# Kernel optimization log

Measured on AMD Instinct MI355X. Metric: run time of the kernel, lower is better.

The kernel has to match this reference:

```python
import jax, jax.numpy as jnp
import numpy as np

NUM_BUOYS = 16384
TIME_STEPS = 8
FEATURE_DIM = 64
ID_EMB_DIM = 1024  # must equal gru_hidden_size for steps 4/5 to type-check
HIDDEN = 1024
NUM_EMB = 100
INPUT_SIZE = FEATURE_DIM + ID_EMB_DIM


def setup_inputs() -> dict:
    key = jax.random.key(0)
    k = jax.random.split(key, 7)
    s = 1.0 / np.sqrt(HIDDEN)
    return {
        "buoy_obs": jax.random.normal(k[0], (NUM_BUOYS, TIME_STEPS, FEATURE_DIM), jnp.float32),
        "buoy_ids": jax.random.randint(k[1], (NUM_BUOYS,), 0, NUM_EMB),
        "emb": jax.random.normal(k[2], (NUM_EMB, ID_EMB_DIM), jnp.float32),
        "W_ih": jax.random.uniform(k[3], (3 * HIDDEN, INPUT_SIZE), jnp.float32, -s, s),
        "W_hh": jax.random.uniform(k[4], (3 * HIDDEN, HIDDEN), jnp.float32, -s, s),
        "b_ih": jax.random.uniform(k[5], (3 * HIDDEN,), jnp.float32, -s, s),
        "b_hh": jax.random.uniform(k[6], (3 * HIDDEN,), jnp.float32, -s, s),
    }


def _gru_cell(x, h, W_ih, W_hh, b_ih, b_hh):
    # PyTorch GRU gate layout: [r, z, n]
    gi = x @ W_ih.T + b_ih  # (N, 3H)
    gh = h @ W_hh.T + b_hh  # (N, 3H)
    gi_r, gi_z, gi_n = jnp.split(gi, 3, axis=-1)
    gh_r, gh_z, gh_n = jnp.split(gh, 3, axis=-1)
    r = jax.nn.sigmoid(gi_r + gh_r)
    z = jax.nn.sigmoid(gi_z + gh_z)
    n = jnp.tanh(gi_n + r * gh_n)
    return (1.0 - z) * n + z * h


def reference(buoy_obs, buoy_ids, emb, W_ih, W_hh, b_ih, b_hh):
    num_buoys = buoy_obs.shape[0]
    id_emb = emb[buoy_ids]  # (N, E)
    h = jnp.zeros((num_buoys, HIDDEN), buoy_obs.dtype)
    outs = []
    # three unrolled steps: input = [obs_t, id_emb]
    for t in range(3):
        x = jnp.concatenate([buoy_obs[:, t, :], id_emb], axis=-1)
        h = _gru_cell(x, h, W_ih, W_hh, b_ih, b_hh)
        outs.append(h)
    # step 4: input = [out0, obs_1]
    x = jnp.concatenate([outs[0], buoy_obs[:, 1, :]], axis=-1)
    h = _gru_cell(x, h, W_ih, W_hh, b_ih, b_hh)
    second_out = h
    # step 5: input = [out4, obs_2]
    x = jnp.concatenate([second_out, buoy_obs[:, 2, :]], axis=-1)
    h = _gru_cell(x, h, W_ih, W_hh, b_ih, b_hh)
    # AdaptiveMaxPool1d(1) over a length-1 time axis is identity
    return h[None, :, :]  # (1, N, H)
```

## Files before the change

### kernel.cpp

```cpp
#include <hip/hip_runtime.h>
#include <hip/hip_bf16.h>


typedef __bf16 bf16_8 __attribute__((ext_vector_type(8)));
typedef float  f32_16 __attribute__((ext_vector_type(16)));

#define NBUOY 16384
#define HID   1024

__device__ __forceinline__ float sigm(float x)  { return 1.f / (1.f + __expf(-x)); }
__device__ __forceinline__ float tanh_f(float x){ return 1.f - 2.f / (1.f + __expf(2.f * x)); }

#define LOADH(a0, a1, br, bz, bn)                                        \
    a0[0] = *(const bf16_8*)(pa0); a0[1] = *(const bf16_8*)(pa0 + 512);  \
    a1[0] = *(const bf16_8*)(pa1); a1[1] = *(const bf16_8*)(pa1 + 512);  \
    br[0] = *(const bf16_8*)(pbr); br[1] = *(const bf16_8*)(pbr + 512);  \
    bz[0] = *(const bf16_8*)(pbz); bz[1] = *(const bf16_8*)(pbz + 512);  \
    bn[0] = *(const bf16_8*)(pbn); bn[1] = *(const bf16_8*)(pbn + 512);  \
    pa0 += 1024; pa1 += 1024; pbr += 1024; pbz += 1024; pbn += 1024;

#define MFMAH(a0, a1, br, bz, bn)                                                         \
    acc[0][0]  = __builtin_amdgcn_mfma_f32_32x32x16_bf16(a0[0], br[0], acc[0][0], 0,0,0); \
    acc[0][1]  = __builtin_amdgcn_mfma_f32_32x32x16_bf16(a1[0], br[0], acc[0][1], 0,0,0); \
    acc[1][0]  = __builtin_amdgcn_mfma_f32_32x32x16_bf16(a0[0], bz[0], acc[1][0], 0,0,0); \
    acc[1][1]  = __builtin_amdgcn_mfma_f32_32x32x16_bf16(a1[0], bz[0], acc[1][1], 0,0,0); \
    acc[QN][0] = __builtin_amdgcn_mfma_f32_32x32x16_bf16(a0[0], bn[0], acc[QN][0],0,0,0); \
    acc[QN][1] = __builtin_amdgcn_mfma_f32_32x32x16_bf16(a1[0], bn[0], acc[QN][1],0,0,0); \
    acc[0][0]  = __builtin_amdgcn_mfma_f32_32x32x16_bf16(a0[1], br[1], acc[0][0], 0,0,0); \
    acc[0][1]  = __builtin_amdgcn_mfma_f32_32x32x16_bf16(a1[1], br[1], acc[0][1], 0,0,0); \
    acc[1][0]  = __builtin_amdgcn_mfma_f32_32x32x16_bf16(a0[1], bz[1], acc[1][0], 0,0,0); \
    acc[1][1]  = __builtin_amdgcn_mfma_f32_32x32x16_bf16(a1[1], bz[1], acc[1][1], 0,0,0); \
    acc[QN][0] = __builtin_amdgcn_mfma_f32_32x32x16_bf16(a0[1], bn[1], acc[QN][0],0,0,0); \
    acc[QN][1] = __builtin_amdgcn_mfma_f32_32x32x16_bf16(a1[1], bn[1], acc[QN][1],0,0,0);

template<int QN, int K>
__device__ __forceinline__ void phase_direct(
    const __bf16* __restrict__ Ap, long aGS, int aG0,
    const __bf16* __restrict__ Wp, long wGS, int n0,
    f32_16 acc[4][2], int tid)
{
    const int lane = tid & 63, wid = tid >> 6;
    const int wm = wid >> 1, wn = wid & 1;
    const int nG = (n0 >> 5) + wn;

    const __bf16* pa0 = Ap + (long)(aG0 + wm * 2    ) * aGS + lane * 8;
    const __bf16* pa1 = Ap + (long)(aG0 + wm * 2 + 1) * aGS + lane * 8;
    const __bf16* pbr = Wp + (long)(      nG) * wGS + lane * 8;
    const __bf16* pbz = Wp + (long)(32  + nG) * wGS + lane * 8;
    const __bf16* pbn = Wp + (long)(64  + nG) * wGS + lane * 8;

    bf16_8 Xa0[2], Xa1[2], Xbr[2], Xbz[2], Xbn[2];
    bf16_8 Ya0[2], Ya1[2], Ybr[2], Ybz[2], Ybn[2];

    constexpr int S = K / 32;
    LOADH(Xa0, Xa1, Xbr, Xbz, Xbn)

    #pragma unroll 1
    for (int s = 0; s + 2 < S; s += 2) {
        LOADH(Ya0, Ya1, Ybr, Ybz, Ybn)
        MFMAH(Xa0, Xa1, Xbr, Xbz, Xbn)
        LOADH(Xa0, Xa1, Xbr, Xbz, Xbn)
        MFMAH(Ya0, Ya1, Ybr, Ybz, Ybn)
    }
    LOADH(Ya0, Ya1, Ybr, Ybz, Ybn)
    MFMAH(Xa0, Xa1, Xbr, Xbz, Xbn)
    MFMAH(Ya0, Ya1, Ybr, Ybz, Ybn)
}

template<int KIH, int KHH, bool USE_E, bool OUT_F32>
__global__ __launch_bounds__(256, 2)
void gru_step(const __bf16* __restrict__ Aih, long aGS,
              const __bf16* __restrict__ Wih,
              const __bf16* __restrict__ Ahh,
              const __bf16* __restrict__ Whh,
              const float*  __restrict__ E,
              const int*    __restrict__ ids,
              const float*  __restrict__ bih,
              const float*  __restrict__ bhh,
              const __bf16* __restrict__ hprev,
              void* __restrict__ outp, long sOut)
{
    const int tid  = threadIdx.x;
    const int lane = tid & 63, wid = tid >> 6;
    const int wm = wid >> 1, wn = wid & 1;
    const int l31 = lane & 31, hi = lane >> 5;
    const int m0 = blockIdx.y * 128;
    const int n0 = blockIdx.x * 64;

    f32_16 acc[4][2];
    #pragma unroll
    for (int q = 0; q < 4; ++q)
        #pragma unroll
        for (int mt = 0; mt < 2; ++mt) acc[q][mt] = (f32_16)(0.0f);

    phase_direct<2, KIH>(Aih, aGS, m0 >> 5, Wih, 34816, n0, acc, tid);
    if (KHH > 0)
        phase_direct<3, KHH>(Ahh, 34816, m0 >> 5, Whh, 32768, n0, acc, tid);

    const int col = n0 + wn * 32 + l31;
    const float bhr = bhh[col], bhz = bhh[1024 + col], bhn = bhh[2048 + col];
    float cir = 0.f, ciz = 0.f, cin = 0.f;
    if (!USE_E) { cir = bih[col]; ciz = bih[1024 + col]; cin = bih[2048 + col]; }
    const long colPk = (long)(col >> 4) * 512 + ((col >> 3) & 1) * 256 + (col & 7);

    #pragma unroll
    for (int mt = 0; mt < 2; ++mt) {
        const int g = (m0 >> 5) + wm * 2 + mt;
        #pragma unroll
        for (int reg = 0; reg < 16; ++reg) {
            const int r = 4 * hi + (reg & 3) + 8 * (reg >> 2);
            const int row = g * 32 + r;
            float er = cir, ez = ciz, en = cin;
            if (USE_E) {
                const float* Ep = E + (long)ids[row] * 3072 + col;
                er = Ep[0]; ez = Ep[1024]; en = Ep[2048];
            }
            const float rr = sigm(acc[0][mt][reg] + er + bhr);
            const float z  = sigm(acc[1][mt][reg] + ez + bhz);
            const float nn = tanh_f(acc[2][mt][reg] + en + rr * (acc[3][mt][reg] + bhn));
            float hp = 0.f;
            if (KHH > 0) hp = (float)hprev[(long)g * 34816 + r * 8 + colPk];
            const float h = (1.f - z) * nn + z * hp;
            if (OUT_F32) ((float*)outp)[(long)row * sOut + col] = h;
            else        ((__bf16*)outp)[(long)g * 34816 + r * 8 + colPk] = (__bf16)h;
        }
    }
}

__global__ void pack_W(const float* __restrict__ W, __bf16* __restrict__ P, int K)
{
    const int q  = blockIdx.x * 256 + threadIdx.x;
    const int kc = q % (K >> 3), row = q / (K >> 3);
    const float4 v0 = *(const float4*)(W + (long)row * K + kc * 8);
    const float4 v1 = *(const float4*)(W + (long)row * K + kc * 8 + 4);
    bf16_8 b;
    b[0] = (__bf16)v0.x; b[1] = (__bf16)v0.y; b[2] = (__bf16)v0.z; b[3] = (__bf16)v0.w;
    b[4] = (__bf16)v1.x; b[5] = (__bf16)v1.y; b[6] = (__bf16)v1.z; b[7] = (__bf16)v1.w;
    const long cidx = (long)(row >> 5) * (K * 4)
                    + (kc >> 1) * 64 + (kc & 1) * 32 + (row & 31);
    ((bf16_8*)P)[cidx] = b;
}

__global__ void build_obs(const float* __restrict__ obs,
                          __bf16* __restrict__ O0, __bf16* __restrict__ O1,
                          __bf16* __restrict__ O2,
                          __bf16* __restrict__ X0, __bf16* __restrict__ X1)
{
    const int q = blockIdx.x * 256 + threadIdx.x;
    const int row = q / 24, c = q % 24;
    const int t = c >> 3, kc = c & 7;
    const float4 v0 = *(const float4*)(obs + (long)row * 512 + t * 64 + kc * 8);
    const float4 v1 = *(const float4*)(obs + (long)row * 512 + t * 64 + kc * 8 + 4);
    bf16_8 b;
    b[0] = (__bf16)v0.x; b[1] = (__bf16)v0.y; b[2] = (__bf16)v0.z; b[3] = (__bf16)v0.w;
    b[4] = (__bf16)v1.x; b[5] = (__bf16)v1.y; b[6] = (__bf16)v1.z; b[7] = (__bf16)v1.w;
    const int g = row >> 5, r = row & 31;
    const long ci = (long)g * 256 + (kc >> 1) * 64 + (kc & 1) * 32 + r;
    __bf16* O = (t == 0) ? O0 : (t == 1) ? O1 : O2;
    ((bf16_8*)O)[ci] = b;
    const long cx = (long)g * 4352 + (64 + (kc >> 1)) * 64 + (kc & 1) * 32 + r;
    if (t == 1) ((bf16_8*)X0)[cx] = b;
    if (t == 2) ((bf16_8*)X1)[cx] = b;
}

#define ETILE 10
__global__ void compute_E(const float* __restrict__ emb, const float* __restrict__ Wih,
                          const float* __restrict__ bih, float* __restrict__ E)
{
    __shared__ float semb[ETILE * 1024];
    const int e0 = blockIdx.x * ETILE;
    const int j  = blockIdx.y * 256 + threadIdx.x;
    for (int i = threadIdx.x; i < ETILE * 1024; i += 256)
        semb[i] = emb[(long)(e0 + (i >> 10)) * 1024 + (i & 1023)];
    __syncthreads();
    const float* wp = Wih + (long)j * 1088 + 64;
    float a[ETILE];
    const float b = bih[j];
    #pragma unroll
    for (int t = 0; t < ETILE; ++t) a[t] = b;
    for (int k = 0; k < 1024; k += 4) {
        const float4 w = *(const float4*)(wp + k);
        #pragma unroll
        for (int t = 0; t < ETILE; ++t) {
            const float* se = semb + t * 1024 + k;
            a[t] += se[0] * w.x + se[1] * w.y + se[2] * w.z + se[3] * w.w;
        }
    }
    #pragma unroll
    for (int t = 0; t < ETILE; ++t) E[(long)(e0 + t) * 3072 + j] = a[t];
}

extern "C" void kernel_launch(void* const* d_in, const int* in_sizes, int n_in,
                              void* d_out, int out_size, void* d_ws, size_t ws_size,
                              hipStream_t stream)
{
    const float* obs = (const float*)d_in[0];
    const int*   ids = (const int*)  d_in[1];
    const float* emb = (const float*)d_in[2];
    const float* Wih = (const float*)d_in[3];
    const float* Whh = (const float*)d_in[4];
    const float* bih = (const float*)d_in[5];
    const float* bhh = (const float*)d_in[6];
    float* out = (float*)d_out;

    const size_t MB = 1 << 20;
    const size_t XB = (size_t)NBUOY * 1088 * 2;
    const size_t NEEDED = 22 * MB + 3 * XB;
    if (ws_size < NEEDED) return;

    char* ws = (char*)d_ws;
    float*  E    = (float*) ws;
    __bf16* PWih = (__bf16*)(ws + 2 * MB);
    __bf16* PWhh = (__bf16*)(ws + 9 * MB);
    __bf16* O0   = (__bf16*)(ws + 16 * MB);
    __bf16* O1   = (__bf16*)(ws + 18 * MB);
    __bf16* O2   = (__bf16*)(ws + 20 * MB);
    __bf16* X0   = (__bf16*)(ws + 22 * MB);
    __bf16* X1   = (__bf16*)(ws + 22 * MB + XB);
    __bf16* X2   = (__bf16*)(ws + 22 * MB + 2 * XB);

    dim3 blk(256);
    dim3 gridG(HID / 64, NBUOY / 128);

    pack_W<<<3072 * 1088 / 8 / 256, blk, 0, stream>>>(Wih, PWih, 1088);
    pack_W<<<3072 * 1024 / 8 / 256, blk, 0, stream>>>(Whh, PWhh, 1024);
    build_obs<<<NBUOY * 24 / 256, blk, 0, stream>>>(obs, O0, O1, O2, X0, X1);
    compute_E<<<dim3(10, 12), blk, 0, stream>>>(emb, Wih, bih, E);

    gru_step<64, 0, true, false><<<gridG, blk, 0, stream>>>(
        O0, 2048, PWih, nullptr, PWhh, E, ids, bih, bhh, nullptr, X0, 0);
    gru_step<64, 1024, true, false><<<gridG, blk, 0, stream>>>(
        O1, 2048, PWih, X0, PWhh, E, ids, bih, bhh, X0, X1, 0);
    gru_step<64, 1024, true, false><<<gridG, blk, 0, stream>>>(
        O2, 2048, PWih, X1, PWhh, E, ids, bih, bhh, X1, X2, 0);
    gru_step<1088, 1024, false, false><<<gridG, blk, 0, stream>>>(
        X0, 34816, PWih, X2, PWhh, nullptr, ids, bih, bhh, X2, X1, 0);
    gru_step<1088, 1024, false, true><<<gridG, blk, 0, stream>>>(
        X1, 34816, PWih, X1, PWhh, nullptr, ids, bih, bhh, X1, out, 1024);
}
```

Measured before the change: 970.7 us.

## Stage GEMM tiles through double-buffered LDS with async loads and larger M tile

Each wave used to load its own A and W fragments straight from global memory into registers. Now each K-slice of the A rows and the three gate weight slices is staged cooperatively into a double-buffered LDS tile using global_load_lds async copies, overlapping the next slice's loads with the current slice's MFMAs. The block grows to 512 threads covering 256 rows instead of 128, so each weight tile is reused across twice as many rows, cutting weight traffic. In exchange the kernel needs about 112 KB of LDS and a barrier per K-slice, which likely limits residency to one block per CU.

```diff
diff --git a/kernel.cpp b/kernel.cpp
--- a/kernel.cpp
+++ b/kernel.cpp
@@ -7,68 +7,70 @@
 
 #define NBUOY 16384
 #define HID   1024
-
+#define BUFSZ 28672
+
+__device__ __forceinline__ void async16(const void* g, void* l) {
+    __builtin_amdgcn_global_load_lds(
+        (const __attribute__((address_space(1))) unsigned int*)g,
+        (__attribute__((address_space(3))) unsigned int*)l, 16, 0, 0);
+}
 __device__ __forceinline__ float sigm(float x)  { return 1.f / (1.f + __expf(-x)); }
 __device__ __forceinline__ float tanh_f(float x){ return 1.f - 2.f / (1.f + __expf(2.f * x)); }
 
-#define LOADH(a0, a1, br, bz, bn)                                        \
-    a0[0] = *(const bf16_8*)(pa0); a0[1] = *(const bf16_8*)(pa0 + 512);  \
-    a1[0] = *(const bf16_8*)(pa1); a1[1] = *(const bf16_8*)(pa1 + 512);  \
-    br[0] = *(const bf16_8*)(pbr); br[1] = *(const bf16_8*)(pbr + 512);  \
-    bz[0] = *(const bf16_8*)(pbz); bz[1] = *(const bf16_8*)(pbz + 512);  \
-    bn[0] = *(const bf16_8*)(pbn); bn[1] = *(const bf16_8*)(pbn + 512);  \
-    pa0 += 1024; pa1 += 1024; pbr += 1024; pbz += 1024; pbn += 1024;
-
-#define MFMAH(a0, a1, br, bz, bn)                                                         \
-    acc[0][0]  = __builtin_amdgcn_mfma_f32_32x32x16_bf16(a0[0], br[0], acc[0][0], 0,0,0); \
-    acc[0][1]  = __builtin_amdgcn_mfma_f32_32x32x16_bf16(a1[0], br[0], acc[0][1], 0,0,0); \
-    acc[1][0]  = __builtin_amdgcn_mfma_f32_32x32x16_bf16(a0[0], bz[0], acc[1][0], 0,0,0); \
-    acc[1][1]  = __builtin_amdgcn_mfma_f32_32x32x16_bf16(a1[0], bz[0], acc[1][1], 0,0,0); \
-    acc[QN][0] = __builtin_amdgcn_mfma_f32_32x32x16_bf16(a0[0], bn[0], acc[QN][0],0,0,0); \
-    acc[QN][1] = __builtin_amdgcn_mfma_f32_32x32x16_bf16(a1[0], bn[0], acc[QN][1],0,0,0); \
-    acc[0][0]  = __builtin_amdgcn_mfma_f32_32x32x16_bf16(a0[1], br[1], acc[0][0], 0,0,0); \
-    acc[0][1]  = __builtin_amdgcn_mfma_f32_32x32x16_bf16(a1[1], br[1], acc[0][1], 0,0,0); \
-    acc[1][0]  = __builtin_amdgcn_mfma_f32_32x32x16_bf16(a0[1], bz[1], acc[1][0], 0,0,0); \
-    acc[1][1]  = __builtin_amdgcn_mfma_f32_32x32x16_bf16(a1[1], bz[1], acc[1][1], 0,0,0); \
-    acc[QN][0] = __builtin_amdgcn_mfma_f32_32x32x16_bf16(a0[1], bn[1], acc[QN][0],0,0,0); \
-    acc[QN][1] = __builtin_amdgcn_mfma_f32_32x32x16_bf16(a1[1], bn[1], acc[QN][1],0,0,0);
-
 template<int QN, int K>
-__device__ __forceinline__ void phase_direct(
+__device__ __forceinline__ void phase_tiled(
     const __bf16* __restrict__ Ap, long aGS, int aG0,
-    const __bf16* __restrict__ Wp, long wGS, int n0,
-    f32_16 acc[4][2], int tid)
+    const __bf16* __restrict__ Wp, long wGS, int nG0,
+    __bf16* ls, f32_16 acc[4][2], int tid, int& buf)
 {
     const int lane = tid & 63, wid = tid >> 6;
     const int wm = wid >> 1, wn = wid & 1;
-    const int nG = (n0 >> 5) + wn;
-
-    const __bf16* pa0 = Ap + (long)(aG0 + wm * 2    ) * aGS + lane * 8;
-    const __bf16* pa1 = Ap + (long)(aG0 + wm * 2 + 1) * aGS + lane * 8;
-    const __bf16* pbr = Wp + (long)(      nG) * wGS + lane * 8;
-    const __bf16* pbz = Wp + (long)(32  + nG) * wGS + lane * 8;
-    const __bf16* pbn = Wp + (long)(64  + nG) * wGS + lane * 8;
-
-    bf16_8 Xa0[2], Xa1[2], Xbr[2], Xbz[2], Xbn[2];
-    bf16_8 Ya0[2], Ya1[2], Ybr[2], Ybz[2], Ybn[2];
-
-    constexpr int S = K / 32;
-    LOADH(Xa0, Xa1, Xbr, Xbz, Xbn)
-
+    constexpr int NT = K / 64;
+
+    auto stage = [&](int b, int t) {
+        __bf16* dst = ls + b * BUFSZ;
+        #pragma unroll
+        for (int i = 0; i < 7; ++i) {
+            const int blk = wid * 7 + i;
+            const __bf16* src;
+            if (blk < 32) {
+                const int g = blk >> 2, kc = blk & 3;
+                src = Ap + (long)(aG0 + g) * aGS + (t * 4 + kc) * 512 + lane * 8;
+            } else {
+                const int u = blk - 32;
+                const int gate = u >> 3, ng = (u >> 2) & 1, kc = u & 3;
+                src = Wp + (long)(gate * 32 + nG0 + ng) * wGS + (t * 4 + kc) * 512 + lane * 8;
+            }
+            async16(src, dst + blk * 512);
+        }
+    };
+
+    stage(buf, 0);
     #pragma unroll 1
-    for (int s = 0; s + 2 < S; s += 2) {
-        LOADH(Ya0, Ya1, Ybr, Ybz, Ybn)
-        MFMAH(Xa0, Xa1, Xbr, Xbz, Xbn)
-        LOADH(Xa0, Xa1, Xbr, Xbz, Xbn)
-        MFMAH(Ya0, Ya1, Ybr, Ybz, Ybn)
+    for (int t = 0; t < NT; ++t) {
+        __syncthreads();
+        if (t + 1 < NT) stage(buf ^ 1, t + 1);
+        const __bf16* base = ls + buf * BUFSZ;
+        #pragma unroll
+        for (int ks = 0; ks < 4; ++ks) {
+            const bf16_8 a0 = *(const bf16_8*)(base + ((wm * 2 + 0) * 4 + ks) * 512 + lane * 8);
+            const bf16_8 a1 = *(const bf16_8*)(base + ((wm * 2 + 1) * 4 + ks) * 512 + lane * 8);
+            const bf16_8 br = *(const bf16_8*)(base + (32 + ((0 * 2 + wn) * 4 + ks)) * 512 + lane * 8);
+            const bf16_8 bz = *(const bf16_8*)(base + (32 + ((1 * 2 + wn) * 4 + ks)) * 512 + lane * 8);
+            const bf16_8 bn = *(const bf16_8*)(base + (32 + ((2 * 2 + wn) * 4 + ks)) * 512 + lane * 8);
+            acc[0][0]  = __builtin_amdgcn_mfma_f32_32x32x16_bf16(a0, br, acc[0][0], 0, 0, 0);
+            acc[0][1]  = __builtin_amdgcn_mfma_f32_32x32x16_bf16(a1, br, acc[0][1], 0, 0, 0);
+            acc[1][0]  = __builtin_amdgcn_mfma_f32_32x32x16_bf16(a0, bz, acc[1][0], 0, 0, 0);
+            acc[1][1]  = __builtin_amdgcn_mfma_f32_32x32x16_bf16(a1, bz, acc[1][1], 0, 0, 0);
+            acc[QN][0] = __builtin_amdgcn_mfma_f32_32x32x16_bf16(a0, bn, acc[QN][0], 0, 0, 0);
+            acc[QN][1] = __builtin_amdgcn_mfma_f32_32x32x16_bf16(a1, bn, acc[QN][1], 0, 0, 0);
+        }
+        buf ^= 1;
     }
-    LOADH(Ya0, Ya1, Ybr, Ybz, Ybn)
-    MFMAH(Xa0, Xa1, Xbr, Xbz, Xbn)
-    MFMAH(Ya0, Ya1, Ybr, Ybz, Ybn)
 }
 
 template<int KIH, int KHH, bool USE_E, bool OUT_F32>
-__global__ __launch_bounds__(256, 2)
+__global__ __launch_bounds__(512, 2)
 void gru_step(const __bf16* __restrict__ Aih, long aGS,
               const __bf16* __restrict__ Wih,
               const __bf16* __restrict__ Ahh,
@@ -80,11 +82,12 @@
               const __bf16* __restrict__ hprev,
               void* __restrict__ outp, long sOut)
 {
+    __shared__ __bf16 ls[2 * BUFSZ];
     const int tid  = threadIdx.x;
     const int lane = tid & 63, wid = tid >> 6;
     const int wm = wid >> 1, wn = wid & 1;
     const int l31 = lane & 31, hi = lane >> 5;
-    const int m0 = blockIdx.y * 128;
+    const int m0 = blockIdx.y * 256;
     const int n0 = blockIdx.x * 64;
 
     f32_16 acc[4][2];
@@ -93,9 +96,10 @@
         #pragma unroll
         for (int mt = 0; mt < 2; ++mt) acc[q][mt] = (f32_16)(0.0f);
 
-    phase_direct<2, KIH>(Aih, aGS, m0 >> 5, Wih, 34816, n0, acc, tid);
+    int buf = 0;
+    phase_tiled<2, KIH>(Aih, aGS, m0 >> 5, Wih, 34816, n0 >> 5, ls, acc, tid, buf);
     if (KHH > 0)
-        phase_direct<3, KHH>(Ahh, 34816, m0 >> 5, Whh, 32768, n0, acc, tid);
+        phase_tiled<3, KHH>(Ahh, 34816, m0 >> 5, Whh, 32768, n0 >> 5, ls, acc, tid, buf);
 
     const int col = n0 + wn * 32 + l31;
     const float bhr = bhh[col], bhz = bhh[1024 + col], bhn = bhh[2048 + col];
@@ -220,21 +224,22 @@
     __bf16* X2   = (__bf16*)(ws + 22 * MB + 2 * XB);
 
     dim3 blk(256);
-    dim3 gridG(HID / 64, NBUOY / 128);
+    dim3 blkG(512);
+    dim3 gridG(HID / 64, NBUOY / 256);
 
     pack_W<<<3072 * 1088 / 8 / 256, blk, 0, stream>>>(Wih, PWih, 1088);
     pack_W<<<3072 * 1024 / 8 / 256, blk, 0, stream>>>(Whh, PWhh, 1024);
     build_obs<<<NBUOY * 24 / 256, blk, 0, stream>>>(obs, O0, O1, O2, X0, X1);
     compute_E<<<dim3(10, 12), blk, 0, stream>>>(emb, Wih, bih, E);
 
-    gru_step<64, 0, true, false><<<gridG, blk, 0, stream>>>(
+    gru_step<64, 0, true, false><<<gridG, blkG, 0, stream>>>(
         O0, 2048, PWih, nullptr, PWhh, E, ids, bih, bhh, nullptr, X0, 0);
-    gru_step<64, 1024, true, false><<<gridG, blk, 0, stream>>>(
+    gru_step<64, 1024, true, false><<<gridG, blkG, 0, stream>>>(
         O1, 2048, PWih, X0, PWhh, E, ids, bih, bhh, X0, X1, 0);
-    gru_step<64, 1024, true, false><<<gridG, blk, 0, stream>>>(
+    gru_step<64, 1024, true, false><<<gridG, blkG, 0, stream>>>(
         O2, 2048, PWih, X1, PWhh, E, ids, bih, bhh, X1, X2, 0);
-    gru_step<1088, 1024, false, false><<<gridG, blk, 0, stream>>>(
+    gru_step<1088, 1024, false, false><<<gridG, blkG, 0, stream>>>(
         X0, 34816, PWih, X2, PWhh, nullptr, ids, bih, bhh, X2, X1, 0);
-    gru_step<1088, 1024, false, true><<<gridG, blk, 0, stream>>>(
+    gru_step<1088, 1024, false, true><<<gridG, blkG, 0, stream>>>(
         X1, 34816, PWih, X1, PWhh, nullptr, ids, bih, bhh, X1, out, 1024);
 }
```

New measurement: 954.6 us. Within noise of the previous version (-1.7%).
